# Kernel tuning notes

Hardware: AMD Instinct MI355X
Metric: run time of the kernel (lower is better)

## Reference

```python
import jax, jax.numpy as jnp
import numpy as np

B, N, D, H = 256, 1000, 128, 8
DH = D // H
TANH_CLIP = 10.0
NEG = -1e9  # finite stand-in for -inf mask fill (keeps grads clean)


def setup_inputs() -> dict:
    key = jax.random.key(0)
    ks = jax.random.split(key, 8)
    s = 1.0 / np.sqrt(D)
    return {
        "node_embeddings": jax.random.normal(ks[0], (B, N, D), jnp.float32),
        "W_node": jax.random.normal(ks[1], (D, 3 * D), jnp.float32) * s,   # project_node_embeddings
        "W_fixed": jax.random.normal(ks[2], (D, D), jnp.float32) * s,      # project_fixed_context
        "W_step": jax.random.normal(ks[3], (2 * D, D), jnp.float32) * s,   # project_step_context
        "W_out": jax.random.normal(ks[4], (D, D), jnp.float32) * s,        # project_out
        "prev_idx": jax.random.randint(ks[5], (B,), 0, N),
        "first_idx": jax.random.randint(ks[6], (B,), 0, N),
        "mask": jax.random.randint(ks[7], (B, N), 0, 2).astype(bool),      # True = masked/visited
    }


def reference(node_embeddings, W_node, W_fixed, W_step, W_out, prev_idx, first_idx, mask):
    b = jnp.arange(B)
    # Precompute fixed: context projection of graph embedding (mean aggregation)
    graph_embed = node_embeddings.mean(axis=1)                    # (B, D)
    fixed_context = graph_embed @ W_fixed                          # (B, D)
    # glimpse key / glimpse val / logit key from node embeddings
    kvl = node_embeddings @ W_node                                 # (B, N, 3D)
    glimpse_K, glimpse_V, logit_K = jnp.split(kvl, 3, axis=-1)
    gK = glimpse_K.reshape(B, N, H, DH)                            # (B, N, H, dh)
    gV = glimpse_V.reshape(B, N, H, DH)
    # Step context: cat(first node embed, last node embed) -> query
    step_ctx = jnp.concatenate(
        [node_embeddings[b, first_idx], node_embeddings[b, prev_idx]], axis=-1)  # (B, 2D)
    query = fixed_context + step_ctx @ W_step                      # (B, D)
    Q = query.reshape(B, H, DH)                                    # (B, H, dh)
    # Glimpse MHA (single query per batch element)
    compat = jnp.einsum("bhd,bnhd->bhn", Q, gK) / np.sqrt(DH)      # (B, H, N)
    compat = jnp.where(mask[:, None, :], NEG, compat)              # mask_inner
    attn = jax.nn.softmax(compat, axis=-1)
    heads = jnp.einsum("bhn,bnhd->bhd", attn, gV)                  # (B, H, dh)
    glimpse = heads.reshape(B, D) @ W_out                          # (B, D)
    # Logits against logit_K, tanh clipping, mask_logits, log-softmax
    logits = jnp.einsum("bd,bnd->bn", glimpse, logit_K) / np.sqrt(D)
    logits = TANH_CLIP * jnp.tanh(logits)
    logits = jnp.where(mask, NEG, logits)
    log_p = jax.nn.log_softmax(logits, axis=-1)                    # (B, N)
    return log_p
```

## Files before the change

kernel.cpp:

```cpp
#include <hip/hip_runtime.h>
#include <math.h>

#define BB 256
#define NN 1000
#define DD 128
#define HH 8
#define NEG -1e9f

__device__ __forceinline__ float bf2f(unsigned int u) {
    return __uint_as_float(u << 16);
}
__device__ __forceinline__ unsigned short f2bf(float f) {
    unsigned int u = __float_as_uint(f);
    u += 0x7FFFu + ((u >> 16) & 1u);
    return (unsigned short)(u >> 16);
}
__device__ __forceinline__ bool get_mask(const void* m, int flag, size_t idx) {
    if (flag == 1) return ((const int*)m)[idx] != 0;
    if (flag == 2) return ((const float*)m)[idx] != 0.0f;
    return ((const unsigned char*)m)[idx] != 0;
}

template<int BF16>
__global__ __launch_bounds__(1024) void k_fused(
        const float* __restrict__ X, const float* __restrict__ Wnode,
        const float* __restrict__ Wfix, const float* __restrict__ Wstep,
        const float* __restrict__ Wout, const int* __restrict__ prev,
        const int* __restrict__ first, const void* __restrict__ mask,
        unsigned short* __restrict__ Xb, float* __restrict__ out) {
    int b = blockIdx.x, tid = threadIdx.x;

    __shared__ __align__(16) float cm[HH * 1024];
    __shared__ __align__(16) float qkl[HH * DD];
    __shared__ __align__(16) float qpart[8 * DD];
    __shared__ float xa[HH * DD];
    __shared__ float ge[DD], q[DD], sc[2 * DD], hd[DD], gl[DD], gqv[DD];
    __shared__ float red[16], invh[8];
    __shared__ int s_flag;

    const size_t xoff = (size_t)b * NN * DD;

    if (tid < 64) {
        const unsigned int* mw = (const unsigned int*)mask;
        unsigned int a0 = mw[tid], a1 = mw[tid + 64], a2 = mw[tid + 128], a3 = mw[tid + 192];
        int ii = (a0 <= 1u) && (a1 <= 1u) && (a2 <= 1u) && (a3 <= 1u);
        int ff = (a0 == 0u || a0 == 0x3F800000u) && (a1 == 0u || a1 == 0x3F800000u) &&
                 (a2 == 0u || a2 == 0x3F800000u) && (a3 == 0u || a3 == 0x3F800000u);
        int ai = __all(ii), af = __all(ff);
        if (tid == 0) s_flag = ai ? 1 : (af ? 2 : 0);
    }
    if (tid >= 256 && tid < 512) {
        int t = tid - 256;
        int src = (t < DD) ? first[b] : prev[b];
        sc[t] = X[xoff + (size_t)src * DD + (t & 127)];
    }

    {
        float4* red4 = (float4*)cm;
        int c = tid & 31, s = tid >> 5;
        const float4* Xr = (const float4*)(X + xoff);
        float4 acc = make_float4(0.f, 0.f, 0.f, 0.f);
        for (int n = s; n < NN; n += 32) {
            float4 v = Xr[n * 32 + c];
            acc.x += v.x; acc.y += v.y; acc.z += v.z; acc.w += v.w;
            if (BF16) {
                uint2 p;
                p.x = (unsigned)f2bf(v.x) | ((unsigned)f2bf(v.y) << 16);
                p.y = (unsigned)f2bf(v.z) | ((unsigned)f2bf(v.w) << 16);
                ((uint2*)Xb)[(size_t)b * NN * 32 + n * 32 + c] = p;
            }
        }
        red4[s * 32 + c] = acc;
        __syncthreads();
        for (int st = 16; st >= 1; st >>= 1) {
            if (s < st) {
                float4 o = red4[(s + st) * 32 + c];
                float4 r = red4[s * 32 + c];
                r.x += o.x; r.y += o.y; r.z += o.z; r.w += o.w;
                red4[s * 32 + c] = r;
            }
            __syncthreads();
        }
        if (s == 0) {
            float4 r = red4[c];
            ge[4 * c]     = r.x * (1.0f / NN);
            ge[4 * c + 1] = r.y * (1.0f / NN);
            ge[4 * c + 2] = r.z * (1.0f / NN);
            ge[4 * c + 3] = r.w * (1.0f / NN);
        }
        __syncthreads();
    }
    const int flag = s_flag;

    {
        int p = tid >> 7, d = tid & 127;
        float a = 0.f;
        #pragma unroll 4
        for (int k = p * 16; k < p * 16 + 16; ++k) a += ge[k] * Wfix[(size_t)k * DD + d];
        #pragma unroll 4
        for (int k = p * 32; k < p * 32 + 32; ++k) a += sc[k] * Wstep[(size_t)k * DD + d];
        qpart[p * DD + d] = a;
        __syncthreads();
        if (tid < DD) {
            float s = 0.f;
            #pragma unroll
            for (int pp = 0; pp < 8; ++pp) s += qpart[pp * DD + tid];
            q[tid] = s;
        }
        __syncthreads();
        int d2 = tid >> 3, h = tid & 7;
        const float4* wr = (const float4*)(Wnode + (size_t)d2 * 384 + h * 16);
        float a2 = 0.f;
        #pragma unroll
        for (int j4 = 0; j4 < 4; ++j4) {
            float4 w = wr[j4];
            a2 += w.x * q[h * 16 + 4 * j4]     + w.y * q[h * 16 + 4 * j4 + 1]
                + w.z * q[h * 16 + 4 * j4 + 2] + w.w * q[h * 16 + 4 * j4 + 3];
        }
        qkl[h * DD + d2] = 0.25f * a2;
        __syncthreads();
    }

    {
        int g = tid & 7;
        for (int it = 0; it < 8; ++it) {
            int n = it * 128 + (tid >> 3);
            if (n < NN) {
                float acc[HH] = {0.f, 0.f, 0.f, 0.f, 0.f, 0.f, 0.f, 0.f};
                if (BF16) {
                    const uint4* xr = (const uint4*)(Xb + xoff + (size_t)n * DD);
                    uint4 c0 = xr[g], c1 = xr[g + 8];
                    unsigned int wsv[8] = {c0.x, c0.y, c0.z, c0.w, c1.x, c1.y, c1.z, c1.w};
                    #pragma unroll
                    for (int i = 0; i < 8; ++i) {
                        int col = (i < 4) ? (8 * g + 2 * i) : (64 + 8 * g + 2 * (i - 4));
                        float lo = bf2f(wsv[i] & 0xffffu), hi = bf2f(wsv[i] >> 16);
                        #pragma unroll
                        for (int h = 0; h < HH; ++h)
                            acc[h] += lo * qkl[h * DD + col] + hi * qkl[h * DD + col + 1];
                    }
                } else {
                    const float4* xr = (const float4*)(X + xoff + (size_t)n * DD);
                    #pragma unroll
                    for (int i = 0; i < 4; ++i) {
                        float4 v = xr[g + 8 * i];
                        int col = 4 * (g + 8 * i);
                        #pragma unroll
                        for (int h = 0; h < HH; ++h)
                            acc[h] += v.x * qkl[h * DD + col]     + v.y * qkl[h * DD + col + 1]
                                    + v.z * qkl[h * DD + col + 2] + v.w * qkl[h * DD + col + 3];
                    }
                }
                #pragma unroll
                for (int h = 0; h < HH; ++h) {
                    acc[h] += __shfl_xor(acc[h], 1, 8);
                    acc[h] += __shfl_xor(acc[h], 2, 8);
                    acc[h] += __shfl_xor(acc[h], 4, 8);
                }
                bool mk = get_mask(mask, flag, (size_t)b * NN + n);
                cm[g * 1024 + n] = mk ? NEG : acc[g];
            }
        }
        __syncthreads();
    }

    {
        int h = tid >> 7, lane = tid & 127;
        float mx = -INFINITY;
        for (int n = lane; n < NN; n += 128) mx = fmaxf(mx, cm[h * 1024 + n]);
        #pragma unroll
        for (int off = 32; off >= 1; off >>= 1) mx = fmaxf(mx, __shfl_xor(mx, off, 64));
        if ((tid & 63) == 0) red[tid >> 6] = mx;
        __syncthreads();
        float m_h = fmaxf(red[2 * h], red[2 * h + 1]);
        float sm = 0.f;
        for (int n = lane; n < NN; n += 128) {
            float p = expf(cm[h * 1024 + n] - m_h);
            cm[h * 1024 + n] = p;
            sm += p;
        }
        #pragma unroll
        for (int off = 32; off >= 1; off >>= 1) sm += __shfl_xor(sm, off, 64);
        __syncthreads();
        if ((tid & 63) == 0) red[tid >> 6] = sm;
        __syncthreads();
        if (tid < HH) invh[tid] = 1.0f / (red[2 * tid] + red[2 * tid + 1]);
        __syncthreads();
    }

    {
        int s = tid >> 7, d = tid & 127;
        float acc[HH] = {0.f, 0.f, 0.f, 0.f, 0.f, 0.f, 0.f, 0.f};
        for (int n = s; n < NN; n += 8) {
            float x = BF16 ? bf2f((unsigned int)Xb[xoff + (size_t)n * DD + d])
                           : X[xoff + (size_t)n * DD + d];
            #pragma unroll
            for (int h = 0; h < HH; ++h) acc[h] += cm[h * 1024 + n] * x;
        }
        __syncthreads();
        float* xp = cm;
        #pragma unroll
        for (int h = 0; h < HH; ++h) xp[(s * HH + h) * DD + d] = acc[h];
        __syncthreads();
        if (s == 0) {
            #pragma unroll
            for (int h = 0; h < HH; ++h) {
                float t = 0.f;
                #pragma unroll
                for (int ss = 0; ss < 8; ++ss) t += xp[(ss * HH + h) * DD + d];
                xa[h * DD + d] = t * invh[h];
            }
        }
        __syncthreads();
    }

    {
        int p = tid >> 7, t = tid & 127;
        int h = t >> 4;
        float a = 0.f;
        #pragma unroll 4
        for (int d = p * 16; d < p * 16 + 16; ++d)
            a += xa[h * DD + d] * Wnode[(size_t)d * 384 + 128 + t];
        qpart[p * DD + t] = a;
        __syncthreads();
        if (tid < DD) {
            float s = 0.f;
            #pragma unroll
            for (int pp = 0; pp < 8; ++pp) s += qpart[pp * DD + tid];
            hd[tid] = s;
        }
        __syncthreads();
        a = 0.f;
        #pragma unroll 4
        for (int k = p * 16; k < p * 16 + 16; ++k) a += hd[k] * Wout[(size_t)k * DD + t];
        qpart[p * DD + t] = a;
        __syncthreads();
        if (tid < DD) {
            float s = 0.f;
            #pragma unroll
            for (int pp = 0; pp < 8; ++pp) s += qpart[pp * DD + tid];
            gl[tid] = s;
        }
        __syncthreads();
        const float4* wr = (const float4*)(Wnode + (size_t)t * 384 + 256 + p * 16);
        a = 0.f;
        #pragma unroll
        for (int j4 = 0; j4 < 4; ++j4) {
            float4 w = wr[j4];
            int k = p * 16 + 4 * j4;
            a += w.x * gl[k] + w.y * gl[k + 1] + w.z * gl[k + 2] + w.w * gl[k + 3];
        }
        qpart[p * DD + t] = a;
        __syncthreads();
        if (tid < DD) {
            float s = 0.f;
            #pragma unroll
            for (int pp = 0; pp < 8; ++pp) s += qpart[pp * DD + tid];
            gqv[tid] = s * 0.08838834764831845f;
        }
        __syncthreads();
    }

    {
        float* lg = qkl;
        int g = tid & 7;
        for (int it = 0; it < 8; ++it) {
            int n = it * 128 + (tid >> 3);
            if (n < NN) {
                float a = 0.f;
                if (BF16) {
                    const uint4* xr = (const uint4*)(Xb + xoff + (size_t)n * DD);
                    uint4 c0 = xr[g], c1 = xr[g + 8];
                    unsigned int wsv[8] = {c0.x, c0.y, c0.z, c0.w, c1.x, c1.y, c1.z, c1.w};
                    #pragma unroll
                    for (int i = 0; i < 8; ++i) {
                        int col = (i < 4) ? (8 * g + 2 * i) : (64 + 8 * g + 2 * (i - 4));
                        a += bf2f(wsv[i] & 0xffffu) * gqv[col] + bf2f(wsv[i] >> 16) * gqv[col + 1];
                    }
                } else {
                    const float4* xr = (const float4*)(X + xoff + (size_t)n * DD);
                    #pragma unroll
                    for (int i = 0; i < 4; ++i) {
                        float4 v = xr[g + 8 * i];
                        int col = 4 * (g + 8 * i);
                        a += v.x * gqv[col] + v.y * gqv[col + 1] + v.z * gqv[col + 2] + v.w * gqv[col + 3];
                    }
                }
                a += __shfl_xor(a, 1, 8);
                a += __shfl_xor(a, 2, 8);
                a += __shfl_xor(a, 4, 8);
                if (g == 0) {
                    float lgt = 10.0f * tanhf(a);
                    lg[n] = get_mask(mask, flag, (size_t)b * NN + n) ? NEG : lgt;
                }
            }
        }
        __syncthreads();
        float v = (tid < NN) ? lg[tid] : -INFINITY;
        float mx = v;
        #pragma unroll
        for (int off = 32; off >= 1; off >>= 1) mx = fmaxf(mx, __shfl_xor(mx, off, 64));
        if ((tid & 63) == 0) red[tid >> 6] = mx;
        __syncthreads();
        float m = red[0];
        #pragma unroll
        for (int w = 1; w < 16; ++w) m = fmaxf(m, red[w]);
        float e = (tid < NN) ? expf(v - m) : 0.f;
        float sm = e;
        #pragma unroll
        for (int off = 32; off >= 1; off >>= 1) sm += __shfl_xor(sm, off, 64);
        __syncthreads();
        if ((tid & 63) == 0) red[tid >> 6] = sm;
        __syncthreads();
        float s2 = 0.f;
        #pragma unroll
        for (int w = 0; w < 16; ++w) s2 += red[w];
        float lse = m + logf(s2);
        if (tid < NN) out[(size_t)b * NN + tid] = v - lse;
    }
}

extern "C" void kernel_launch(void* const* d_in, const int* in_sizes, int n_in,
                              void* d_out, int out_size, void* d_ws, size_t ws_size,
                              hipStream_t stream) {
    const float* X     = (const float*)d_in[0];
    const float* Wnode = (const float*)d_in[1];
    const float* Wfix  = (const float*)d_in[2];
    const float* Wstep = (const float*)d_in[3];
    const float* Wout  = (const float*)d_in[4];
    const int*   prev  = (const int*)d_in[5];
    const int*   first = (const int*)d_in[6];
    const void*  mask  = d_in[7];
    float* out = (float*)d_out;

    const size_t need = 256 + (size_t)2 * BB * NN * DD;
    if (ws_size >= need) {
        unsigned short* Xb = (unsigned short*)((char*)d_ws + 256);
        k_fused<1><<<BB, 1024, 0, stream>>>(X, Wnode, Wfix, Wstep, Wout,
                                            prev, first, mask, Xb, out);
    } else {
        k_fused<0><<<BB, 1024, 0, stream>>>(X, Wnode, Wfix, Wstep, Wout,
                                            prev, first, mask, nullptr, out);
    }
}
```

Before: 109.4 us.

## Split fused decoder into split-N multi-kernel pipeline with flash-style softmax combine

Replaces the single per-batch 1024-thread fused kernel with six kernels. The mean, attention and logit passes each split N into 8 chunks, so 2048 blocks run instead of 256. Attention uses per-chunk max and sum partials that a combine kernel merges. The log-softmax uses the fixed bound of the tanh-clipped logits (10) as its shift, which avoids a global max pass. The bf16 workspace copy of X is dropped, so every pass reads fp32 X: more memory traffic and extra launches, in exchange for much better occupancy and parallelism.

```diff
diff --git a/kernel.cpp b/kernel.cpp
--- a/kernel.cpp
+++ b/kernel.cpp
@@ -5,31 +5,339 @@
 #define NN 1000
 #define DD 128
 #define HH 8
+#define CC 8
+#define RC 125
 #define NEG -1e9f
 
-__device__ __forceinline__ float bf2f(unsigned int u) {
-    return __uint_as_float(u << 16);
-}
-__device__ __forceinline__ unsigned short f2bf(float f) {
-    unsigned int u = __float_as_uint(f);
-    u += 0x7FFFu + ((u >> 16) & 1u);
-    return (unsigned short)(u >> 16);
-}
 __device__ __forceinline__ bool get_mask(const void* m, int flag, size_t idx) {
     if (flag == 1) return ((const int*)m)[idx] != 0;
     if (flag == 2) return ((const float*)m)[idx] != 0.0f;
     return ((const unsigned char*)m)[idx] != 0;
 }
 
-template<int BF16>
-__global__ __launch_bounds__(1024) void k_fused(
+__global__ __launch_bounds__(256) void k_mean(
+        const float* __restrict__ X, float* __restrict__ partial,
+        const unsigned int* __restrict__ maskw, int* __restrict__ flag) {
+    int bid = blockIdx.x, tid = threadIdx.x;
+    int b = bid >> 3, ch = bid & 7;
+    if (bid == 0 && tid < 64) {
+        unsigned int a0 = maskw[tid], a1 = maskw[tid + 64],
+                     a2 = maskw[tid + 128], a3 = maskw[tid + 192];
+        int ii = (a0 <= 1u) && (a1 <= 1u) && (a2 <= 1u) && (a3 <= 1u);
+        int ff = (a0 == 0u || a0 == 0x3F800000u) && (a1 == 0u || a1 == 0x3F800000u) &&
+                 (a2 == 0u || a2 == 0x3F800000u) && (a3 == 0u || a3 == 0x3F800000u);
+        int ai = __all(ii), af = __all(ff);
+        if (tid == 0) *flag = ai ? 1 : (af ? 2 : 0);
+    }
+    int c = tid & 31, s = tid >> 5;
+    const float4* Xr = (const float4*)(X + (size_t)b * NN * DD);
+    float4 acc = make_float4(0.f, 0.f, 0.f, 0.f);
+    int n0 = ch * RC;
+    for (int nl = s; nl < RC; nl += 8) {
+        float4 v = Xr[(n0 + nl) * 32 + c];
+        acc.x += v.x; acc.y += v.y; acc.z += v.z; acc.w += v.w;
+    }
+    __shared__ float4 red[8][32];
+    red[s][c] = acc;
+    __syncthreads();
+    for (int st = 4; st >= 1; st >>= 1) {
+        if (s < st) {
+            float4 o = red[s + st][c];
+            red[s][c].x += o.x; red[s][c].y += o.y;
+            red[s][c].z += o.z; red[s][c].w += o.w;
+        }
+        __syncthreads();
+    }
+    if (s == 0) {
+        float4 r = red[0][c];
+        float* outp = partial + ((size_t)b * CC + ch) * DD + 4 * c;
+        outp[0] = r.x; outp[1] = r.y; outp[2] = r.z; outp[3] = r.w;
+    }
+}
+
+__global__ __launch_bounds__(256) void k_qk(
+        const float* __restrict__ X, const float* __restrict__ Wfix,
+        const float* __restrict__ Wstep, const float* __restrict__ Wnode,
+        const float* __restrict__ partial, const int* __restrict__ prev,
+        const int* __restrict__ first, float* __restrict__ qkg) {
+    int b = blockIdx.x, tid = threadIdx.x;
+    const size_t xoff = (size_t)b * NN * DD;
+    __shared__ float ge[DD], sc[2 * DD], qv[DD], qp[2][DD];
+    if (tid < DD) {
+        float g = 0.f;
+        #pragma unroll
+        for (int ch = 0; ch < CC; ++ch) g += partial[((size_t)b * CC + ch) * DD + tid];
+        ge[tid] = g * (1.0f / NN);
+    }
+    {
+        int src = (tid < DD) ? first[b] : prev[b];
+        sc[tid] = X[xoff + (size_t)src * DD + (tid & 127)];
+    }
+    __syncthreads();
+    int p = tid >> 7, d = tid & 127;
+    {
+        float a = 0.f;
+        #pragma unroll 4
+        for (int k = p * 64; k < p * 64 + 64; ++k)      a += ge[k] * Wfix[(size_t)k * DD + d];
+        #pragma unroll 4
+        for (int k = p * 128; k < p * 128 + 128; ++k)   a += sc[k] * Wstep[(size_t)k * DD + d];
+        qp[p][d] = a;
+    }
+    __syncthreads();
+    if (tid < DD) qv[tid] = qp[0][tid] + qp[1][tid];
+    __syncthreads();
+    {
+        const float* wrow = Wnode + (size_t)d * 384;
+        #pragma unroll
+        for (int h = p * 4; h < p * 4 + 4; ++h) {
+            const float4* wr = (const float4*)(wrow + h * 16);
+            float a = 0.f;
+            #pragma unroll
+            for (int j4 = 0; j4 < 4; ++j4) {
+                float4 w = wr[j4];
+                a += w.x * qv[h * 16 + 4 * j4]     + w.y * qv[h * 16 + 4 * j4 + 1]
+                   + w.z * qv[h * 16 + 4 * j4 + 2] + w.w * qv[h * 16 + 4 * j4 + 3];
+            }
+            qkg[((size_t)b * HH + h) * DD + d] = 0.25f * a;
+        }
+    }
+}
+
+__global__ __launch_bounds__(256, 8) void k_flash(
+        const float* __restrict__ X, const float* __restrict__ qkg,
+        const void* __restrict__ mask, const int* __restrict__ flag,
+        float* __restrict__ mqw, float* __restrict__ sqw,
+        float* __restrict__ pvp) {
+    int bid = blockIdx.x, tid = threadIdx.x;
+    int b = bid >> 3, ch = bid & 7;
+    const int n0 = ch * RC;
+    const size_t xoff = (size_t)b * NN * DD;
+    const int f = *flag;
+
+    __shared__ float qk[HH][DD];
+    __shared__ float cm[HH][RC + 3];
+    __shared__ float mloc[HH];
+    __shared__ float xp[2][HH][DD];
+
+    for (int i = tid; i < HH * DD; i += 256)
+        qk[i >> 7][i & 127] = qkg[(size_t)b * HH * DD + i];
+    __syncthreads();
+
+    {
+        int g = tid & 7, r = tid >> 3;
+        #pragma unroll
+        for (int it = 0; it < 4; ++it) {
+            int nl = it * 32 + r;
+            if (it < 3 || nl < RC) {
+                int n = n0 + nl;
+                const float4* xr = (const float4*)(X + xoff + (size_t)n * DD);
+                float acc[HH] = {0.f, 0.f, 0.f, 0.f, 0.f, 0.f, 0.f, 0.f};
+                #pragma unroll
+                for (int i = 0; i < 4; ++i) {
+                    float4 v = xr[g + 8 * i];
+                    int col = 4 * (g + 8 * i);
+                    #pragma unroll
+                    for (int h = 0; h < HH; ++h)
+                        acc[h] += v.x * qk[h][col]     + v.y * qk[h][col + 1]
+                                + v.z * qk[h][col + 2] + v.w * qk[h][col + 3];
+                }
+                #pragma unroll
+                for (int h = 0; h < HH; ++h) {
+                    acc[h] += __shfl_xor(acc[h], 1, 8);
+                    acc[h] += __shfl_xor(acc[h], 2, 8);
+                    acc[h] += __shfl_xor(acc[h], 4, 8);
+                }
+                float val = acc[0];
+                #pragma unroll
+                for (int h = 1; h < HH; ++h) val = (g == h) ? acc[h] : val;
+                bool mk = get_mask(mask, f, (size_t)b * NN + n);
+                cm[g][nl] = mk ? NEG : val;
+            }
+        }
+    }
+    __syncthreads();
+
+    {
+        int h = tid >> 5, l = tid & 31;
+        float mx = -INFINITY;
+        for (int nl = l; nl < RC; nl += 32) mx = fmaxf(mx, cm[h][nl]);
+        #pragma unroll
+        for (int off = 16; off >= 1; off >>= 1) mx = fmaxf(mx, __shfl_xor(mx, off, 32));
+        if (l == 0) mloc[h] = mx;
+    }
+    __syncthreads();
+
+    {
+        int h = tid >> 5, l = tid & 31;
+        float m_h = mloc[h];
+        float sm = 0.f;
+        for (int nl = l; nl < RC; nl += 32) {
+            float p = __expf(cm[h][nl] - m_h);
+            cm[h][nl] = p;
+            sm += p;
+        }
+        #pragma unroll
+        for (int off = 16; off >= 1; off >>= 1) sm += __shfl_xor(sm, off, 32);
+        if (l == 0) {
+            sqw[((size_t)b * CC + ch) * HH + h] = sm;
+            mqw[((size_t)b * CC + ch) * HH + h] = m_h;
+        }
+    }
+    __syncthreads();
+
+    {
+        int s2 = tid >> 7, d = tid & 127;
+        float acc[HH] = {0.f, 0.f, 0.f, 0.f, 0.f, 0.f, 0.f, 0.f};
+        #pragma unroll 2
+        for (int nl = s2; nl < RC; nl += 2) {
+            float x = X[xoff + (size_t)(n0 + nl) * DD + d];
+            #pragma unroll
+            for (int h = 0; h < HH; ++h) acc[h] += cm[h][nl] * x;
+        }
+        #pragma unroll
+        for (int h = 0; h < HH; ++h) xp[s2][h][d] = acc[h];
+        __syncthreads();
+        if (s2 == 0) {
+            #pragma unroll
+            for (int h = 0; h < HH; ++h)
+                pvp[(((size_t)b * CC + ch) * HH + h) * DD + d] = xp[0][h][d] + xp[1][h][d];
+        }
+    }
+}
+
+__global__ __launch_bounds__(256) void k_comb(
+        const float* __restrict__ Wnode, const float* __restrict__ Wout,
+        const float* __restrict__ mqw, const float* __restrict__ sqw,
+        const float* __restrict__ pvp, float* __restrict__ gqg) {
+    int b = blockIdx.x, tid = threadIdx.x;
+    __shared__ float wq[CC][HH], Sh[HH];
+    __shared__ float xa[HH][DD], qp[2][DD], hd[DD], gl[DD];
+    if (tid < HH) {
+        float m = mqw[((size_t)b * CC) * HH + tid];
+        #pragma unroll
+        for (int ch = 1; ch < CC; ++ch)
+            m = fmaxf(m, mqw[((size_t)b * CC + ch) * HH + tid]);
+        float S = 0.f;
+        #pragma unroll
+        for (int ch = 0; ch < CC; ++ch) {
+            float wgt = __expf(mqw[((size_t)b * CC + ch) * HH + tid] - m);
+            wq[ch][tid] = wgt;
+            S += sqw[((size_t)b * CC + ch) * HH + tid] * wgt;
+        }
+        Sh[tid] = 1.0f / S;
+    }
+    __syncthreads();
+    for (int idx = tid; idx < HH * DD; idx += 256) {
+        int h = idx >> 7, d = idx & 127;
+        float a = 0.f;
+        #pragma unroll
+        for (int ch = 0; ch < CC; ++ch)
+            a += pvp[(((size_t)b * CC + ch) * HH + h) * DD + d] * wq[ch][h];
+        xa[h][d] = a * Sh[h];
+    }
+    __syncthreads();
+    int p = tid >> 7, t = tid & 127;
+    {
+        int h = t >> 4;
+        float a = 0.f;
+        #pragma unroll 4
+        for (int d = p * 64; d < p * 64 + 64; ++d)
+            a += xa[h][d] * Wnode[(size_t)d * 384 + 128 + t];
+        qp[p][t] = a;
+    }
+    __syncthreads();
+    if (tid < DD) hd[tid] = qp[0][tid] + qp[1][tid];
+    __syncthreads();
+    {
+        float a = 0.f;
+        #pragma unroll 4
+        for (int k = p * 64; k < p * 64 + 64; ++k) a += hd[k] * Wout[(size_t)k * DD + t];
+        qp[p][t] = a;
+    }
+    __syncthreads();
+    if (tid < DD) gl[tid] = qp[0][tid] + qp[1][tid];
+    __syncthreads();
+    {
+        const float4* wr = (const float4*)(Wnode + (size_t)t * 384 + 256 + p * 64);
+        float a = 0.f;
+        #pragma unroll
+        for (int j4 = 0; j4 < 16; ++j4) {
+            float4 w = wr[j4];
+            int k = p * 64 + 4 * j4;
+            a += w.x * gl[k] + w.y * gl[k + 1] + w.z * gl[k + 2] + w.w * gl[k + 3];
+        }
+        qp[p][t] = a;
+    }
+    __syncthreads();
+    if (tid < DD) gqg[(size_t)b * DD + tid] = (qp[0][tid] + qp[1][tid]) * 0.08838834764831845f;
+}
+
+__global__ __launch_bounds__(256, 8) void k_logits(
+        const float* __restrict__ X, const float* __restrict__ gqg,
+        const void* __restrict__ mask, const int* __restrict__ flag,
+        float* __restrict__ lg, float* __restrict__ esumg) {
+    int bid = blockIdx.x, tid = threadIdx.x;
+    int b = bid >> 3, ch = bid & 7;
+    const int n0 = ch * RC;
+    const size_t xoff = (size_t)b * NN * DD;
+    const int f = *flag;
+    __shared__ float gqv[DD];
+    __shared__ float redw[4];
+    if (tid < DD) gqv[tid] = gqg[(size_t)b * DD + tid];
+    __syncthreads();
+    int g = tid & 7, r = tid >> 3;
+    float esum = 0.f;
+    #pragma unroll
+    for (int it = 0; it < 4; ++it) {
+        int nl = it * 32 + r;
+        if (it < 3 || nl < RC) {
+            int n = n0 + nl;
+            const float4* xr = (const float4*)(X + xoff + (size_t)n * DD);
+            float a = 0.f;
+            #pragma unroll
+            for (int i = 0; i < 4; ++i) {
+                float4 v = xr[g + 8 * i];
+                int col = 4 * (g + 8 * i);
+                a += v.x * gqv[col] + v.y * gqv[col + 1]
+                   + v.z * gqv[col + 2] + v.w * gqv[col + 3];
+            }
+            a += __shfl_xor(a, 1, 8);
+            a += __shfl_xor(a, 2, 8);
+            a += __shfl_xor(a, 4, 8);
+            if (g == 0) {
+                float l = 10.0f * tanhf(a);
+                if (get_mask(mask, f, (size_t)b * NN + n)) l = NEG;
+                lg[(size_t)b * NN + n] = l;
+                esum += __expf(l - 10.0f);
+            }
+        }
+    }
+    #pragma unroll
+    for (int off = 32; off >= 1; off >>= 1) esum += __shfl_xor(esum, off, 64);
+    if ((tid & 63) == 0) redw[tid >> 6] = esum;
+    __syncthreads();
+    if (tid == 0) esumg[(size_t)b * CC + ch] = redw[0] + redw[1] + redw[2] + redw[3];
+}
+
+__global__ __launch_bounds__(256) void k_final(
+        const float* __restrict__ lg, const float* __restrict__ esumg,
+        float* __restrict__ out) {
+    int b = blockIdx.x, tid = threadIdx.x;
+    float s = 0.f;
+    #pragma unroll
+    for (int ch = 0; ch < CC; ++ch) s += esumg[(size_t)b * CC + ch];
+    float lse = 10.0f + logf(s);
+    for (int n = tid; n < NN; n += 256)
+        out[(size_t)b * NN + n] = lg[(size_t)b * NN + n] - lse;
+}
+
+__global__ __launch_bounds__(1024) void k_mega(
         const float* __restrict__ X, const float* __restrict__ Wnode,
         const float* __restrict__ Wfix, const float* __restrict__ Wstep,
         const float* __restrict__ Wout, const int* __restrict__ prev,
         const int* __restrict__ first, const void* __restrict__ mask,
-        unsigned short* __restrict__ Xb, float* __restrict__ out) {
+        float* __restrict__ out) {
     int b = blockIdx.x, tid = threadIdx.x;
-
     __shared__ __align__(16) float cm[HH * 1024];
     __shared__ __align__(16) float qkl[HH * DD];
     __shared__ __align__(16) float qpart[8 * DD];
@@ -37,7 +345,6 @@
     __shared__ float ge[DD], q[DD], sc[2 * DD], hd[DD], gl[DD], gqv[DD];
     __shared__ float red[16], invh[8];
     __shared__ int s_flag;
-
     const size_t xoff = (size_t)b * NN * DD;
 
     if (tid < 64) {
@@ -54,7 +361,6 @@
         int src = (t < DD) ? first[b] : prev[b];
         sc[t] = X[xoff + (size_t)src * DD + (t & 127)];
     }
-
     {
         float4* red4 = (float4*)cm;
         int c = tid & 31, s = tid >> 5;
@@ -63,12 +369,6 @@
         for (int n = s; n < NN; n += 32) {
             float4 v = Xr[n * 32 + c];
             acc.x += v.x; acc.y += v.y; acc.z += v.z; acc.w += v.w;
-            if (BF16) {
-                uint2 p;
-                p.x = (unsigned)f2bf(v.x) | ((unsigned)f2bf(v.y) << 16);
-                p.y = (unsigned)f2bf(v.z) | ((unsigned)f2bf(v.w) << 16);
-                ((uint2*)Xb)[(size_t)b * NN * 32 + n * 32 + c] = p;
-            }
         }
         red4[s * 32 + c] = acc;
         __syncthreads();
@@ -83,27 +383,21 @@
         }
         if (s == 0) {
             float4 r = red4[c];
-            ge[4 * c]     = r.x * (1.0f / NN);
-            ge[4 * c + 1] = r.y * (1.0f / NN);
-            ge[4 * c + 2] = r.z * (1.0f / NN);
-            ge[4 * c + 3] = r.w * (1.0f / NN);
+            ge[4 * c] = r.x * (1.0f / NN); ge[4 * c + 1] = r.y * (1.0f / NN);
+            ge[4 * c + 2] = r.z * (1.0f / NN); ge[4 * c + 3] = r.w * (1.0f / NN);
         }
         __syncthreads();
     }
     const int flag = s_flag;
-
     {
         int p = tid >> 7, d = tid & 127;
         float a = 0.f;
-        #pragma unroll 4
-        for (int k = p * 16; k < p * 16 + 16; ++k) a += ge[k] * Wfix[(size_t)k * DD + d];
-        #pragma unroll 4
-        for (int k = p * 32; k < p * 32 + 32; ++k) a += sc[k] * Wstep[(size_t)k * DD + d];
+        for (int k = p * 16; k < p * 16 + 16; ++k) a += ge[k] * Wfix[k * DD + d];
+        for (int k = p * 32; k < p * 32 + 32; ++k) a += sc[k] * Wstep[k * DD + d];
         qpart[p * DD + d] = a;
         __syncthreads();
         if (tid < DD) {
             float s = 0.f;
-            #pragma unroll
             for (int pp = 0; pp < 8; ++pp) s += qpart[pp * DD + tid];
             q[tid] = s;
         }
@@ -111,7 +405,6 @@
         int d2 = tid >> 3, h = tid & 7;
         const float4* wr = (const float4*)(Wnode + (size_t)d2 * 384 + h * 16);
         float a2 = 0.f;
-        #pragma unroll
         for (int j4 = 0; j4 < 4; ++j4) {
             float4 w = wr[j4];
             a2 += w.x * q[h * 16 + 4 * j4]     + w.y * q[h * 16 + 4 * j4 + 1]
@@ -120,66 +413,47 @@
         qkl[h * DD + d2] = 0.25f * a2;
         __syncthreads();
     }
-
     {
         int g = tid & 7;
         for (int it = 0; it < 8; ++it) {
             int n = it * 128 + (tid >> 3);
             if (n < NN) {
                 float acc[HH] = {0.f, 0.f, 0.f, 0.f, 0.f, 0.f, 0.f, 0.f};
-                if (BF16) {
-                    const uint4* xr = (const uint4*)(Xb + xoff + (size_t)n * DD);
-                    uint4 c0 = xr[g], c1 = xr[g + 8];
-                    unsigned int wsv[8] = {c0.x, c0.y, c0.z, c0.w, c1.x, c1.y, c1.z, c1.w};
-                    #pragma unroll
-                    for (int i = 0; i < 8; ++i) {
-                        int col = (i < 4) ? (8 * g + 2 * i) : (64 + 8 * g + 2 * (i - 4));
-                        float lo = bf2f(wsv[i] & 0xffffu), hi = bf2f(wsv[i] >> 16);
-                        #pragma unroll
-                        for (int h = 0; h < HH; ++h)
-                            acc[h] += lo * qkl[h * DD + col] + hi * qkl[h * DD + col + 1];
-                    }
-                } else {
-                    const float4* xr = (const float4*)(X + xoff + (size_t)n * DD);
-                    #pragma unroll
-                    for (int i = 0; i < 4; ++i) {
-                        float4 v = xr[g + 8 * i];
-                        int col = 4 * (g + 8 * i);
-                        #pragma unroll
-                        for (int h = 0; h < HH; ++h)
-                            acc[h] += v.x * qkl[h * DD + col]     + v.y * qkl[h * DD + col + 1]
-                                    + v.z * qkl[h * DD + col + 2] + v.w * qkl[h * DD + col + 3];
-                    }
+                const float4* xr = (const float4*)(X + xoff + (size_t)n * DD);
+                for (int i = 0; i < 4; ++i) {
+                    float4 v = xr[g + 8 * i];
+                    int col = 4 * (g + 8 * i);
+                    for (int h = 0; h < HH; ++h)
+                        acc[h] += v.x * qkl[h * DD + col]     + v.y * qkl[h * DD + col + 1]
+                                + v.z * qkl[h * DD + col + 2] + v.w * qkl[h * DD + col + 3];
                 }
-                #pragma unroll
                 for (int h = 0; h < HH; ++h) {
                     acc[h] += __shfl_xor(acc[h], 1, 8);
                     acc[h] += __shfl_xor(acc[h], 2, 8);
                     acc[h] += __shfl_xor(acc[h], 4, 8);
                 }
+                float val = acc[0];
+                for (int h = 1; h < HH; ++h) val = (g == h) ? acc[h] : val;
                 bool mk = get_mask(mask, flag, (size_t)b * NN + n);
-                cm[g * 1024 + n] = mk ? NEG : acc[g];
-            }
-        }
-        __syncthreads();
-    }
-
+                cm[g * 1024 + n] = mk ? NEG : val;
+            }
+        }
+        __syncthreads();
+    }
     {
         int h = tid >> 7, lane = tid & 127;
         float mx = -INFINITY;
         for (int n = lane; n < NN; n += 128) mx = fmaxf(mx, cm[h * 1024 + n]);
-        #pragma unroll
         for (int off = 32; off >= 1; off >>= 1) mx = fmaxf(mx, __shfl_xor(mx, off, 64));
         if ((tid & 63) == 0) red[tid >> 6] = mx;
         __syncthreads();
         float m_h = fmaxf(red[2 * h], red[2 * h + 1]);
         float sm = 0.f;
         for (int n = lane; n < NN; n += 128) {
-            float p = expf(cm[h * 1024 + n] - m_h);
+            float p = __expf(cm[h * 1024 + n] - m_h);
             cm[h * 1024 + n] = p;
             sm += p;
         }
-        #pragma unroll
         for (int off = 32; off >= 1; off >>= 1) sm += __shfl_xor(sm, off, 64);
         __syncthreads();
         if ((tid & 63) == 0) red[tid >> 6] = sm;
@@ -187,64 +461,52 @@
         if (tid < HH) invh[tid] = 1.0f / (red[2 * tid] + red[2 * tid + 1]);
         __syncthreads();
     }
-
     {
         int s = tid >> 7, d = tid & 127;
         float acc[HH] = {0.f, 0.f, 0.f, 0.f, 0.f, 0.f, 0.f, 0.f};
         for (int n = s; n < NN; n += 8) {
-            float x = BF16 ? bf2f((unsigned int)Xb[xoff + (size_t)n * DD + d])
-                           : X[xoff + (size_t)n * DD + d];
-            #pragma unroll
+            float x = X[xoff + (size_t)n * DD + d];
             for (int h = 0; h < HH; ++h) acc[h] += cm[h * 1024 + n] * x;
         }
         __syncthreads();
         float* xp = cm;
-        #pragma unroll
         for (int h = 0; h < HH; ++h) xp[(s * HH + h) * DD + d] = acc[h];
         __syncthreads();
         if (s == 0) {
-            #pragma unroll
             for (int h = 0; h < HH; ++h) {
                 float t = 0.f;
-                #pragma unroll
                 for (int ss = 0; ss < 8; ++ss) t += xp[(ss * HH + h) * DD + d];
                 xa[h * DD + d] = t * invh[h];
             }
         }
         __syncthreads();
     }
-
     {
         int p = tid >> 7, t = tid & 127;
         int h = t >> 4;
         float a = 0.f;
-        #pragma unroll 4
         for (int d = p * 16; d < p * 16 + 16; ++d)
             a += xa[h * DD + d] * Wnode[(size_t)d * 384 + 128 + t];
         qpart[p * DD + t] = a;
         __syncthreads();
         if (tid < DD) {
             float s = 0.f;
-            #pragma unroll
             for (int pp = 0; pp < 8; ++pp) s += qpart[pp * DD + tid];
             hd[tid] = s;
         }
         __syncthreads();
         a = 0.f;
-        #pragma unroll 4
         for (int k = p * 16; k < p * 16 + 16; ++k) a += hd[k] * Wout[(size_t)k * DD + t];
         qpart[p * DD + t] = a;
         __syncthreads();
         if (tid < DD) {
             float s = 0.f;
-            #pragma unroll
             for (int pp = 0; pp < 8; ++pp) s += qpart[pp * DD + tid];
             gl[tid] = s;
         }
         __syncthreads();
         const float4* wr = (const float4*)(Wnode + (size_t)t * 384 + 256 + p * 16);
         a = 0.f;
-        #pragma unroll
         for (int j4 = 0; j4 < 4; ++j4) {
             float4 w = wr[j4];
             int k = p * 16 + 4 * j4;
@@ -254,37 +516,23 @@
         __syncthreads();
         if (tid < DD) {
             float s = 0.f;
-            #pragma unroll
             for (int pp = 0; pp < 8; ++pp) s += qpart[pp * DD + tid];
             gqv[tid] = s * 0.08838834764831845f;
         }
         __syncthreads();
     }
-
     {
         float* lg = qkl;
         int g = tid & 7;
         for (int it = 0; it < 8; ++it) {
             int n = it * 128 + (tid >> 3);
             if (n < NN) {
+                const float4* xr = (const float4*)(X + xoff + (size_t)n * DD);
                 float a = 0.f;
-                if (BF16) {
-                    const uint4* xr = (const uint4*)(Xb + xoff + (size_t)n * DD);
-                    uint4 c0 = xr[g], c1 = xr[g + 8];
-                    unsigned int wsv[8] = {c0.x, c0.y, c0.z, c0.w, c1.x, c1.y, c1.z, c1.w};
-                    #pragma unroll
-                    for (int i = 0; i < 8; ++i) {
-                        int col = (i < 4) ? (8 * g + 2 * i) : (64 + 8 * g + 2 * (i - 4));
-                        a += bf2f(wsv[i] & 0xffffu) * gqv[col] + bf2f(wsv[i] >> 16) * gqv[col + 1];
-                    }
-                } else {
-                    const float4* xr = (const float4*)(X + xoff + (size_t)n * DD);
-                    #pragma unroll
-                    for (int i = 0; i < 4; ++i) {
-                        float4 v = xr[g + 8 * i];
-                        int col = 4 * (g + 8 * i);
-                        a += v.x * gqv[col] + v.y * gqv[col + 1] + v.z * gqv[col + 2] + v.w * gqv[col + 3];
-                    }
+                for (int i = 0; i < 4; ++i) {
+                    float4 v = xr[g + 8 * i];
+                    int col = 4 * (g + 8 * i);
+                    a += v.x * gqv[col] + v.y * gqv[col + 1] + v.z * gqv[col + 2] + v.w * gqv[col + 3];
                 }
                 a += __shfl_xor(a, 1, 8);
                 a += __shfl_xor(a, 2, 8);
@@ -298,22 +546,18 @@
         __syncthreads();
         float v = (tid < NN) ? lg[tid] : -INFINITY;
         float mx = v;
-        #pragma unroll
         for (int off = 32; off >= 1; off >>= 1) mx = fmaxf(mx, __shfl_xor(mx, off, 64));
         if ((tid & 63) == 0) red[tid >> 6] = mx;
         __syncthreads();
         float m = red[0];
-        #pragma unroll
         for (int w = 1; w < 16; ++w) m = fmaxf(m, red[w]);
-        float e = (tid < NN) ? expf(v - m) : 0.f;
+        float e = (tid < NN) ? __expf(v - m) : 0.f;
         float sm = e;
-        #pragma unroll
         for (int off = 32; off >= 1; off >>= 1) sm += __shfl_xor(sm, off, 64);
         __syncthreads();
         if ((tid & 63) == 0) red[tid >> 6] = sm;
         __syncthreads();
         float s2 = 0.f;
-        #pragma unroll
         for (int w = 0; w < 16; ++w) s2 += red[w];
         float lse = m + logf(s2);
         if (tid < NN) out[(size_t)b * NN + tid] = v - lse;
@@ -333,13 +577,30 @@
     const void*  mask  = d_in[7];
     float* out = (float*)d_out;
 
-    const size_t need = 256 + (size_t)2 * BB * NN * DD;
+    char* wsb = (char*)d_ws;
+    int*   flag    = (int*)wsb;
+    float* base    = (float*)(wsb + 256);
+    float* partial = base;
+    float* qkg     = partial + (size_t)BB * CC * DD;
+    float* mqw     = qkg + (size_t)BB * HH * DD;
+    float* sqw     = mqw + (size_t)BB * CC * HH;
+    float* pvp     = sqw + (size_t)BB * CC * HH;
+    float* gqg     = pvp + (size_t)BB * CC * HH * DD;
+    float* esumg   = gqg + (size_t)BB * DD;
+    float* lg      = esumg + (size_t)BB * CC;
+    const size_t need = 256 + sizeof(float) * (
+        (size_t)BB * CC * DD + (size_t)BB * HH * DD + 2 * (size_t)BB * CC * HH +
+        (size_t)BB * CC * HH * DD + (size_t)BB * DD + (size_t)BB * CC + (size_t)BB * NN);
+
     if (ws_size >= need) {
-        unsigned short* Xb = (unsigned short*)((char*)d_ws + 256);
-        k_fused<1><<<BB, 1024, 0, stream>>>(X, Wnode, Wfix, Wstep, Wout,
-                                            prev, first, mask, Xb, out);
+        k_mean  <<<BB * CC, 256, 0, stream>>>(X, partial, (const unsigned int*)mask, flag);
+        k_qk    <<<BB, 256, 0, stream>>>(X, Wfix, Wstep, Wnode, partial, prev, first, qkg);
+        k_flash <<<BB * CC, 256, 0, stream>>>(X, qkg, mask, flag, mqw, sqw, pvp);
+        k_comb  <<<BB, 256, 0, stream>>>(Wnode, Wout, mqw, sqw, pvp, gqg);
+        k_logits<<<BB * CC, 256, 0, stream>>>(X, gqg, mask, flag, lg, esumg);
+        k_final <<<BB, 256, 0, stream>>>(lg, esumg, out);
     } else {
-        k_fused<0><<<BB, 1024, 0, stream>>>(X, Wnode, Wfix, Wstep, Wout,
-                                            prev, first, mask, nullptr, out);
-    }
-}
+        k_mega<<<BB, 1024, 0, stream>>>(X, Wnode, Wfix, Wstep, Wout,
+                                        prev, first, mask, out);
+    }
+}
```

Result: slower. 125.9 us (+15.1%).
